# Optimization experiments

Hardware: AMD Instinct MI355X
Metric: run time of the kernel (lower is better)

## Reference

```python
import jax, jax.numpy as jnp
import numpy as np
import math

B, TQ, TK, C, H, DFF = 4, 1024, 1024, 1024, 16, 4096
DK = C // H
EPS = 1e-12


def _mha(x_q, x_kv, wq, bq, wk, bk, wv, bv, wo, bo, mask):
    Bq, Tq, Cq = x_q.shape
    Tk = x_kv.shape[1]
    q = (x_q @ wq + bq).reshape(Bq, Tq, H, DK).transpose(0, 2, 1, 3)  # [B,H,Tq,dk]
    k = (x_kv @ wk + bk).reshape(Bq, Tk, H, DK).transpose(0, 2, 1, 3)
    v = (x_kv @ wv + bv).reshape(Bq, Tk, H, DK).transpose(0, 2, 1, 3)
    scores = jnp.einsum('bhqd,bhkd->bhqk', q, k) * (1.0 / math.sqrt(DK))
    if mask is not None:
        scores = jnp.where(mask, scores, jnp.asarray(-1e9, scores.dtype))
    attn = jax.nn.softmax(scores, axis=-1)
    o = jnp.einsum('bhqk,bhkd->bhqd', attn, v).transpose(0, 2, 1, 3).reshape(Bq, Tq, Cq)
    return o @ wo + bo


def _ln(x, g, b):
    mu = jnp.mean(x, axis=-1, keepdims=True)
    var = jnp.mean(jnp.square(x - mu), axis=-1, keepdims=True)
    return (x - mu) * jax.lax.rsqrt(var + EPS) * g + b


def setup_inputs() -> dict:
    key = jax.random.key(0)
    ks = iter(jax.random.split(key, 32))
    s = 0.02
    inp = {}
    inp['src'] = jax.random.normal(next(ks), (B, TK, C), jnp.float32)
    inp['dst'] = jax.random.normal(next(ks), (B, TQ, C), jnp.float32)
    inp['src_mask'] = jnp.ones((B, 1, 1, TK), dtype=bool)  # key-padding mask (all valid)
    inp['dst_mask'] = jnp.tril(jnp.ones((TQ, TQ), dtype=bool))[None, None]  # causal
    for p in ['sa', 'ca']:
        for n in ['wq', 'wk', 'wv', 'wo']:
            inp[f'{p}_{n}'] = jax.random.normal(next(ks), (C, C), jnp.float32) * s
        for n in ['bq', 'bk', 'bv', 'bo']:
            inp[f'{p}_{n}'] = jnp.zeros((C,), jnp.float32)
    inp['ffn_w1'] = jax.random.normal(next(ks), (C, DFF), jnp.float32) * s
    inp['ffn_b1'] = jnp.zeros((DFF,), jnp.float32)
    inp['ffn_w2'] = jax.random.normal(next(ks), (DFF, C), jnp.float32) * s
    inp['ffn_b2'] = jnp.zeros((C,), jnp.float32)
    for i in ['1', '2', '3']:
        inp[f'ln{i}_g'] = jnp.ones((C,), jnp.float32)
        inp[f'ln{i}_b'] = jnp.zeros((C,), jnp.float32)
    return inp


def reference(src, dst, src_mask, dst_mask,
              sa_wq, sa_wk, sa_wv, sa_wo, sa_bq, sa_bk, sa_bv, sa_bo,
              ca_wq, ca_wk, ca_wv, ca_wo, ca_bq, ca_bk, ca_bv, ca_bo,
              ffn_w1, ffn_b1, ffn_w2, ffn_b2,
              ln1_g, ln1_b, ln2_g, ln2_b, ln3_g, ln3_b):
    # post-LN decoder layer, eval mode (dropout is identity)
    sa = _mha(dst, dst, sa_wq, sa_bq, sa_wk, sa_bk, sa_wv, sa_bv, sa_wo, sa_bo, dst_mask)
    y = _ln(dst + sa, ln1_g, ln1_b)
    ca = _mha(y, src, ca_wq, ca_bq, ca_wk, ca_bk, ca_wv, ca_bv, ca_wo, ca_bo, src_mask)
    y = _ln(y + ca, ln2_g, ln2_b)
    ff = jax.nn.gelu(y @ ffn_w1 + ffn_b1, approximate=False) @ ffn_w2 + ffn_b2
    return _ln(y + ff, ln3_g, ln3_b)
```

## Files before the change

### kernel.cpp

```cpp
#include <hip/hip_runtime.h>
#include <math.h>

typedef __attribute__((ext_vector_type(4))) float f32x4;
typedef __attribute__((ext_vector_type(8))) __bf16 bf16x8;
typedef __attribute__((ext_vector_type(8))) short short8;

#define DEV __device__ __forceinline__

DEV short f2bfs(float f) {
    unsigned u = __builtin_bit_cast(unsigned, f);
    unsigned r = (u + 0x7FFFu + ((u >> 16) & 1u)) >> 16;
    return (short)r;
}

DEV f32x4 mfma16(bf16x8 a, bf16x8 b, f32x4 c) {
    return __builtin_amdgcn_mfma_f32_16x16x32_bf16(a, b, c, 0, 0, 0);
}

DEV void gload_lds16(const void* g, void* l) {
    __builtin_amdgcn_global_load_lds((const __attribute__((address_space(1))) void*)g,
                                     (__attribute__((address_space(3))) void*)l, 16, 0, 0);
}

__global__ __launch_bounds__(256) void wtrans(const float* __restrict__ Win,
                                              short* __restrict__ Wout,
                                              int Kd, int Nd) {
    __shared__ float Tt[32][33];
    const int tx = threadIdx.x & 31, ty = threadIdx.x >> 5;
    const int k0 = blockIdx.y * 32, n0 = blockIdx.x * 32;
#pragma unroll
    for (int rr = 0; rr < 4; ++rr) {
        int k = ty * 4 + rr;
        Tt[k][tx] = Win[(size_t)(k0 + k) * Nd + n0 + tx];
    }
    __syncthreads();
#pragma unroll
    for (int rr = 0; rr < 4; ++rr) {
        int n = ty * 4 + rr;
        Wout[(size_t)(n0 + n) * Kd + k0 + tx] = f2bfs(Tt[tx][n]);
    }
}

struct WPtrs { const float* p[8]; };

__global__ __launch_bounds__(256) void wtrans8(WPtrs wp, short* __restrict__ out) {
    const float* __restrict__ Win = wp.p[blockIdx.z];
    short* __restrict__ Wout = out + (size_t)blockIdx.z * (1024 * 1024);
    __shared__ float Tt[32][33];
    const int tx = threadIdx.x & 31, ty = threadIdx.x >> 5;
    const int k0 = blockIdx.y * 32, n0 = blockIdx.x * 32;
#pragma unroll
    for (int rr = 0; rr < 4; ++rr) {
        int k = ty * 4 + rr;
        Tt[k][tx] = Win[(size_t)(k0 + k) * 1024 + n0 + tx];
    }
    __syncthreads();
#pragma unroll
    for (int rr = 0; rr < 4; ++rr) {
        int n = ty * 4 + rr;
        Wout[(size_t)(n0 + n) * 1024 + k0 + tx] = f2bfs(Tt[tx][n]);
    }
}

__global__ __launch_bounds__(256) void conv_bf16(const float* __restrict__ X,
                                                 short* __restrict__ Y, int n4) {
    int i = blockIdx.x * 256 + threadIdx.x;
    if (i < n4) {
        float4 v = ((const float4*)X)[i];
        short4 o;
        o.x = f2bfs(v.x); o.y = f2bfs(v.y); o.z = f2bfs(v.z); o.w = f2bfs(v.w);
        ((short4*)Y)[i] = o;
    }
}

template <int BM, int EPI>
__global__ __launch_bounds__(256) void gemm_bt(const short* __restrict__ A,
                                               const short* __restrict__ BT,
                                               const float* __restrict__ b0,
                                               const float* __restrict__ b1,
                                               const float* __restrict__ b2,
                                               void* __restrict__ o0,
                                               void* __restrict__ o1,
                                               void* __restrict__ o2,
                                               int M, int N, int K) {
    constexpr int IM = BM / 32;
    __shared__ __align__(16) short As[2][BM * 32];
    __shared__ __align__(16) short Bs[2][128 * 32];
    const int tid = threadIdx.x, lane = tid & 63, w = tid >> 6;
    const int m0 = blockIdx.y * BM, n0 = blockIdx.x * 128;
    const int wm = (w & 1) * (BM / 2), wn = (w >> 1) * 64;
    const int rl = lane & 15, rg = lane >> 4;
    f32x4 acc[IM][4] = {};
    const char* Ab = (const char*)A;
    const char* Bb = (const char*)BT;
    const int nk = K >> 5;

    auto stage = [&](int kt, int buf) {
#pragma unroll
        for (int r = 0; r < BM / 64; ++r) {
            int lo = (tid + r * 256) * 16;
            int row = lo >> 6, cp = (lo >> 4) & 3, c = (cp - row) & 3;
            gload_lds16(Ab + ((size_t)(m0 + row) * K + kt * 32 + c * 8) * 2,
                        (char*)As[buf] + lo);
        }
#pragma unroll
        for (int r = 0; r < 2; ++r) {
            int lo = (tid + r * 256) * 16;
            int row = lo >> 6, cp = (lo >> 4) & 3, c = (cp - row) & 3;
            gload_lds16(Bb + ((size_t)(n0 + row) * K + kt * 32 + c * 8) * 2,
                        (char*)Bs[buf] + lo);
        }
    };

    stage(0, 0);
    for (int kt = 0; kt < nk; ++kt) {
        const int buf = kt & 1;
        __syncthreads();
        if (kt + 1 < nk) stage(kt + 1, buf ^ 1);
        bf16x8 af[IM], bfr[4];
#pragma unroll
        for (int i = 0; i < IM; i++) {
            int row = wm + i * 16 + rl;
            af[i] = *(const bf16x8*)(As[buf] + row * 32 + ((rg + row) & 3) * 8);
        }
#pragma unroll
        for (int j = 0; j < 4; j++) {
            int row = wn + j * 16 + rl;
            bfr[j] = *(const bf16x8*)(Bs[buf] + row * 32 + ((rg + row) & 3) * 8);
        }
#pragma unroll
        for (int i = 0; i < IM; i++)
#pragma unroll
            for (int j = 0; j < 4; j++)
                acc[i][j] = mfma16(af[i], bfr[j], acc[i][j]);
    }

#pragma unroll
    for (int i = 0; i < IM; i++) {
        int gm0 = m0 + wm + i * 16 + rg * 4;
#pragma unroll
        for (int j = 0; j < 4; j++) {
            int gn = n0 + wn + j * 16 + rl;
            if (EPI == 0) {
                float bv = b0[gn];
#pragma unroll
                for (int r = 0; r < 4; r++)
                    ((float*)o0)[(size_t)(gm0 + r) * N + gn] = acc[i][j][r] + bv;
            } else if (EPI == 2) {
                float bv = b0[gn];
#pragma unroll
                for (int r = 0; r < 4; r++) {
                    float x = acc[i][j][r] + bv;
                    float z = 1.59576912f * x + 0.07135481f * x * x * x;
                    float g = x / (1.0f + __expf(-z));
                    ((short*)o0)[(size_t)(gm0 + r) * N + gn] = f2bfs(g);
                }
            } else {
                int seg = gn >> 10, n1 = gn & 1023, h = n1 >> 6, d = n1 & 63;
                int b = gm0 >> 10, t0 = gm0 & 1023;
                bool isV = (EPI == 1) ? (seg == 2) : (seg == 1);
                const float* bp = (EPI == 1) ? (seg == 0 ? b0 : (seg == 1 ? b1 : b2))
                                             : (seg == 0 ? b0 : b1);
                float bv = bp[n1];
                float qs = (EPI == 1 && seg == 0) ? 0.125f : 1.0f;
                if (!isV) {
                    short* hp = (short*)((EPI == 1) ? (seg == 0 ? o0 : o1) : o0);
                    size_t base = ((size_t)(b * 16 + h) * 1024 + t0) * 64 + d;
#pragma unroll
                    for (int r = 0; r < 4; r++)
                        hp[base + (size_t)r * 64] = f2bfs((acc[i][j][r] + bv) * qs);
                } else {
                    short* vp = (short*)((EPI == 1) ? o2 : o1);
                    short4 pk;
                    pk.x = f2bfs(acc[i][j][0] + bv);
                    pk.y = f2bfs(acc[i][j][1] + bv);
                    pk.z = f2bfs(acc[i][j][2] + bv);
                    pk.w = f2bfs(acc[i][j][3] + bv);
                    *(short4*)(vp + ((size_t)(b * 16 + h) * 64 + d) * 1024 + t0) = pk;
                }
            }
        }
    }
}

template <bool CAUSAL>
__global__ __launch_bounds__(256, 3) void attn4(const short* __restrict__ Qh,
                                                const short* __restrict__ Kh,
                                                const short* __restrict__ VTh,
                                                short* __restrict__ Out, int TKn) {
    __shared__ __align__(16) short Ks[2][64 * 64];
    __shared__ __align__(16) short Vts[2][64 * 64];
    __shared__ __align__(16) short Ps[4][16 * 72 + 8];
    const int tid = threadIdx.x, lane = tid & 63, w = tid >> 6;
    const int rl = lane & 15, rg = lane >> 4;
    const int bh = blockIdx.y, b = bh >> 4, h = bh & 15;
    const int q0 = blockIdx.x * 64;
    const short* Qp = Qh + (size_t)bh * 1024 * 64;
    const char* Kp = (const char*)(Kh + (size_t)bh * (size_t)TKn * 64);
    const char* Vp = (const char*)(VTh + (size_t)bh * (size_t)TKn * 64);

    const int qrow = q0 + w * 16 + rl;
    const bf16x8 qf0 = *(const bf16x8*)(Qp + (size_t)qrow * 64 + rg * 8);
    const bf16x8 qf1 = *(const bf16x8*)(Qp + (size_t)qrow * 64 + 32 + rg * 8);

    bf16x8 onesf;
#pragma unroll
    for (int i = 0; i < 8; ++i) onesf[i] = (__bf16)1.0f;

    f32x4 o[4] = {};
    f32x4 lacc = {};

    short* Pw = &Ps[w][0];
    const int nkt = CAUSAL ? blockIdx.x + 1 : (TKn >> 6);

    auto stage = [&](int kt, int buf) {
#pragma unroll
        for (int r = 0; r < 2; ++r) {
            int lo = (w * 2 + r) * 1024 + lane * 16;
            int row = lo >> 7, cp = (lo >> 4) & 7, c = (cp - row) & 7;
            gload_lds16(Kp + ((size_t)(kt * 64 + row) * 64 + c * 8) * 2,
                        (char*)Ks[buf] + lo);
            gload_lds16(Vp + ((size_t)row * TKn + kt * 64 + c * 8) * 2,
                        (char*)Vts[buf] + lo);
        }
    };

    stage(0, 0);
    for (int kt = 0; kt < nkt; ++kt) {
        const int buf = kt & 1;
        __syncthreads();
        if (kt + 1 < nkt) stage(kt + 1, buf ^ 1);

        const short* KsB = Ks[buf];
        f32x4 s[4];
#pragma unroll
        for (int ch = 0; ch < 4; ++ch) {
            int row = ch * 16 + rl;
            bf16x8 k0 = *(const bf16x8*)(KsB + row * 64 + ((rg + row) & 7) * 8);
            bf16x8 k1 = *(const bf16x8*)(KsB + row * 64 + ((rg + 4 + row) & 7) * 8);
            f32x4 z = {};
            z = mfma16(k0, qf0, z);
            z = mfma16(k1, qf1, z);
            s[ch] = z;
        }
        const bool domask = CAUSAL && (kt == nkt - 1);
#pragma unroll
        for (int ch = 0; ch < 4; ++ch) {
            float p[4];
#pragma unroll
            for (int r = 0; r < 4; ++r) {
                float e = __expf(s[ch][r]);
                if (domask) {
                    int key = kt * 64 + ch * 16 + rg * 4 + r;
                    if (key > qrow) e = 0.0f;
                }
                p[r] = e;
            }
            unsigned d0 = (__builtin_bit_cast(unsigned, p[1]) & 0xFFFF0000u) |
                          (__builtin_bit_cast(unsigned, p[0]) >> 16);
            unsigned d1 = (__builtin_bit_cast(unsigned, p[3]) & 0xFFFF0000u) |
                          (__builtin_bit_cast(unsigned, p[2]) >> 16);
            uint2 dv; dv.x = d0; dv.y = d1;
            *(uint2*)(Pw + rl * 72 + ch * 16 + rg * 4) = dv;
        }
        bf16x8 pa0 = *(const bf16x8*)(Pw + rl * 72 + rg * 8);
        bf16x8 pa1 = *(const bf16x8*)(Pw + rl * 72 + 32 + rg * 8);
        lacc = mfma16(pa0, onesf, lacc);
        lacc = mfma16(pa1, onesf, lacc);
        const short* VsB = Vts[buf];
#pragma unroll
        for (int j = 0; j < 4; ++j) {
            int row = j * 16 + rl;
            bf16x8 v0 = *(const bf16x8*)(VsB + row * 64 + ((rg + row) & 7) * 8);
            bf16x8 v1 = *(const bf16x8*)(VsB + row * 64 + ((rg + 4 + row) & 7) * 8);
            o[j] = mfma16(pa0, v0, o[j]);
            o[j] = mfma16(pa1, v1, o[j]);
        }
    }

    float inv[4];
#pragma unroll
    for (int r = 0; r < 4; r++) inv[r] = 1.0f / lacc[r];
#pragma unroll
    for (int j = 0; j < 4; j++) {
#pragma unroll
        for (int r = 0; r < 4; r++) {
            int row = q0 + w * 16 + rg * 4 + r;
            int col = h * 64 + j * 16 + rl;
            Out[((size_t)b * 1024 + row) * 1024 + col] = f2bfs(o[j][r] * inv[r]);
        }
    }
}

__global__ __launch_bounds__(256) void ln_fused(const float* __restrict__ X,
                                                const float* __restrict__ R,
                                                const float* __restrict__ gam,
                                                const float* __restrict__ bet,
                                                float* __restrict__ Yf,
                                                short* __restrict__ Yb) {
    const int row = blockIdx.x, tid = threadIdx.x;
    const int lane = tid & 63, w = tid >> 6;
    const float* xr = X + (size_t)row * 1024;
    const float* rr = R + (size_t)row * 1024;
    float4 xv = ((const float4*)xr)[tid];
    float4 rv = ((const float4*)rr)[tid];
    float v0 = xv.x + rv.x, v1 = xv.y + rv.y, v2 = xv.z + rv.z, v3 = xv.w + rv.w;
    float s = v0 + v1 + v2 + v3;
    float ss = v0 * v0 + v1 * v1 + v2 * v2 + v3 * v3;
#pragma unroll
    for (int off = 1; off < 64; off <<= 1) {
        s += __shfl_xor(s, off);
        ss += __shfl_xor(ss, off);
    }
    __shared__ float sred[4], ssred[4];
    if (lane == 0) { sred[w] = s; ssred[w] = ss; }
    __syncthreads();
    s = sred[0] + sred[1] + sred[2] + sred[3];
    ss = ssred[0] + ssred[1] + ssred[2] + ssred[3];
    float mu = s * (1.0f / 1024.0f);
    float var = ss * (1.0f / 1024.0f) - mu * mu;
    float rsq = rsqrtf(var + 1e-12f);
    float4 gv = ((const float4*)gam)[tid];
    float4 bv = ((const float4*)bet)[tid];
    float y0 = (v0 - mu) * rsq * gv.x + bv.x;
    float y1 = (v1 - mu) * rsq * gv.y + bv.y;
    float y2 = (v2 - mu) * rsq * gv.z + bv.z;
    float y3 = (v3 - mu) * rsq * gv.w + bv.w;
    float4 yo = {y0, y1, y2, y3};
    ((float4*)(Yf + (size_t)row * 1024))[tid] = yo;
    if (Yb) {
        short4 ob;
        ob.x = f2bfs(y0); ob.y = f2bfs(y1); ob.z = f2bfs(y2); ob.w = f2bfs(y3);
        ((short4*)(Yb + (size_t)row * 1024))[tid] = ob;
    }
}

extern "C" void kernel_launch(void* const* d_in, const int* in_sizes, int n_in,
                              void* d_out, int out_size, void* d_ws, size_t ws_size,
                              hipStream_t stream) {
    const float* src = (const float*)d_in[0];
    const float* dst = (const float*)d_in[1];
    const float* sa_wq = (const float*)d_in[4];
    const float* sa_wk = (const float*)d_in[5];
    const float* sa_wv = (const float*)d_in[6];
    const float* sa_wo = (const float*)d_in[7];
    const float* sa_bq = (const float*)d_in[8];
    const float* sa_bk = (const float*)d_in[9];
    const float* sa_bv = (const float*)d_in[10];
    const float* sa_bo = (const float*)d_in[11];
    const float* ca_wq = (const float*)d_in[12];
    const float* ca_wk = (const float*)d_in[13];
    const float* ca_wv = (const float*)d_in[14];
    const float* ca_wo = (const float*)d_in[15];
    const float* ca_bq = (const float*)d_in[16];
    const float* ca_bk = (const float*)d_in[17];
    const float* ca_bv = (const float*)d_in[18];
    const float* ca_bo = (const float*)d_in[19];
    const float* ffn_w1 = (const float*)d_in[20];
    const float* ffn_b1 = (const float*)d_in[21];
    const float* ffn_w2 = (const float*)d_in[22];
    const float* ffn_b2 = (const float*)d_in[23];
    const float* ln1g = (const float*)d_in[24];
    const float* ln1b = (const float*)d_in[25];
    const float* ln2g = (const float*)d_in[26];
    const float* ln2b = (const float*)d_in[27];
    const float* ln3g = (const float*)d_in[28];
    const float* ln3b = (const float*)d_in[29];

    char* ws = (char*)d_ws;
    size_t off = 0;
    auto alloc = [&](size_t n) { size_t o = off; off = (off + n + 255) & ~(size_t)255; return o; };

    const size_t szW = (size_t)1024 * 1024 * 2;
    short* wT = (short*)(ws + alloc(8 * szW));
    short* w1T = (short*)(ws + alloc((size_t)4096 * 1024 * 2));
    short* w2T = (short*)(ws + alloc((size_t)1024 * 4096 * 2));
    const size_t szAct2 = (size_t)4096 * 1024 * 2;
    const size_t szAct4 = (size_t)4096 * 1024 * 4;
    short* dstb = (short*)(ws + alloc(szAct2));
    short* srcb = (short*)(ws + alloc(szAct2));
    short* Qh = (short*)(ws + alloc(szAct2));
    short* Kh = (short*)(ws + alloc(szAct2));
    short* VTh = (short*)(ws + alloc(szAct2));
    short* attnb = (short*)(ws + alloc(szAct2));
    float* tmp = (float*)(ws + alloc(szAct4));
    float* y1f = (float*)(ws + alloc(szAct4));
    short* y1b = (short*)(ws + alloc(szAct2));
    float* y2f = (float*)(ws + alloc(szAct4));
    short* y2b = (short*)(ws + alloc(szAct2));
    short* ffnh = (short*)(ws + alloc((size_t)4096 * 4096 * 2));

    short* sa_wqkvT = wT;
    short* sa_woT = wT + 3 * (size_t)1048576;
    short* ca_wqT = wT + 4 * (size_t)1048576;
    short* ca_wkvT = wT + 5 * (size_t)1048576;
    short* ca_woT = wT + 7 * (size_t)1048576;

    dim3 blk(256);

    WPtrs wp = {{sa_wq, sa_wk, sa_wv, sa_wo, ca_wq, ca_wk, ca_wv, ca_wo}};
    wtrans8<<<dim3(32, 32, 8), blk, 0, stream>>>(wp, wT);
    wtrans<<<dim3(128, 32), blk, 0, stream>>>(ffn_w1, w1T, 1024, 4096);
    wtrans<<<dim3(32, 128), blk, 0, stream>>>(ffn_w2, w2T, 4096, 1024);
    conv_bf16<<<4096, blk, 0, stream>>>(dst, dstb, 1048576);
    conv_bf16<<<4096, blk, 0, stream>>>(src, srcb, 1048576);

    gemm_bt<128, 1><<<dim3(24, 32), blk, 0, stream>>>(dstb, sa_wqkvT, sa_bq, sa_bk, sa_bv,
                                                      Qh, Kh, VTh, 4096, 3072, 1024);
    attn4<true><<<dim3(16, 64), blk, 0, stream>>>(Qh, Kh, VTh, attnb, 1024);
    gemm_bt<64, 0><<<dim3(8, 64), blk, 0, stream>>>(attnb, sa_woT, sa_bo, nullptr, nullptr,
                                                    tmp, nullptr, nullptr, 4096, 1024, 1024);
    ln_fused<<<4096, blk, 0, stream>>>(dst, tmp, ln1g, ln1b, y1f, y1b);

    gemm_bt<64, 1><<<dim3(8, 64), blk, 0, stream>>>(y1b, ca_wqT, ca_bq, nullptr, nullptr,
                                                    Qh, nullptr, nullptr, 4096, 1024, 1024);
    gemm_bt<128, 3><<<dim3(16, 32), blk, 0, stream>>>(srcb, ca_wkvT, ca_bk, ca_bv, nullptr,
                                                      Kh, VTh, nullptr, 4096, 2048, 1024);
    attn4<false><<<dim3(16, 64), blk, 0, stream>>>(Qh, Kh, VTh, attnb, 1024);
    gemm_bt<64, 0><<<dim3(8, 64), blk, 0, stream>>>(attnb, ca_woT, ca_bo, nullptr, nullptr,
                                                    tmp, nullptr, nullptr, 4096, 1024, 1024);
    ln_fused<<<4096, blk, 0, stream>>>(y1f, tmp, ln2g, ln2b, y2f, y2b);

    gemm_bt<128, 2><<<dim3(32, 32), blk, 0, stream>>>(y2b, w1T, ffn_b1, nullptr, nullptr,
                                                      ffnh, nullptr, nullptr, 4096, 4096, 1024);
    gemm_bt<64, 0><<<dim3(8, 64), blk, 0, stream>>>(ffnh, w2T, ffn_b2, nullptr, nullptr,
                                                    tmp, nullptr, nullptr, 4096, 1024, 4096);
    ln_fused<<<4096, blk, 0, stream>>>(y2f, tmp, ln3g, ln3b, (float*)d_out, nullptr);

    (void)in_sizes; (void)n_in; (void)out_size; (void)ws_size;
}
```

Measured before the change: 544.1 us.

## Split-K the N=1024 output GEMMs and fold partial sums into LayerNorm

The three output-projection GEMMs (N=1024) now run with a two-way split over K via blockIdx.z. Each half writes its partial result to a separate fp32 buffer, and the bias is added only in the first half. The following LayerNorm kernel reads both partials and sums them into the residual, so no separate reduction kernel is needed. This doubles the block count for GEMMs that launched only 512 blocks, to fill more CUs, at the cost of writing and reading an extra fp32 activation buffer. The LDS swizzle also changes from (row) to (row>>1), which alters the bank-conflict pattern of the tile loads and reads.

```diff
diff --git a/kernel.cpp b/kernel.cpp
--- a/kernel.cpp
+++ b/kernel.cpp
@@ -82,12 +82,13 @@
                                                void* __restrict__ o0,
                                                void* __restrict__ o1,
                                                void* __restrict__ o2,
-                                               int M, int N, int K) {
+                                               int M, int N, int K, int Ks) {
     constexpr int IM = BM / 32;
     __shared__ __align__(16) short As[2][BM * 32];
     __shared__ __align__(16) short Bs[2][128 * 32];
     const int tid = threadIdx.x, lane = tid & 63, w = tid >> 6;
     const int m0 = blockIdx.y * BM, n0 = blockIdx.x * 128;
+    const int kz = blockIdx.z * K;
     const int wm = (w & 1) * (BM / 2), wn = (w >> 1) * 64;
     const int rl = lane & 15, rg = lane >> 4;
     f32x4 acc[IM][4] = {};
@@ -99,15 +100,15 @@
 #pragma unroll
         for (int r = 0; r < BM / 64; ++r) {
             int lo = (tid + r * 256) * 16;
-            int row = lo >> 6, cp = (lo >> 4) & 3, c = (cp - row) & 3;
-            gload_lds16(Ab + ((size_t)(m0 + row) * K + kt * 32 + c * 8) * 2,
+            int row = lo >> 6, cp = (lo >> 4) & 3, c = (cp - (row >> 1)) & 3;
+            gload_lds16(Ab + ((size_t)(m0 + row) * Ks + kz + kt * 32 + c * 8) * 2,
                         (char*)As[buf] + lo);
         }
 #pragma unroll
         for (int r = 0; r < 2; ++r) {
             int lo = (tid + r * 256) * 16;
-            int row = lo >> 6, cp = (lo >> 4) & 3, c = (cp - row) & 3;
-            gload_lds16(Bb + ((size_t)(n0 + row) * K + kt * 32 + c * 8) * 2,
+            int row = lo >> 6, cp = (lo >> 4) & 3, c = (cp - (row >> 1)) & 3;
+            gload_lds16(Bb + ((size_t)(n0 + row) * Ks + kz + kt * 32 + c * 8) * 2,
                         (char*)Bs[buf] + lo);
         }
     };
@@ -121,12 +122,12 @@
 #pragma unroll
         for (int i = 0; i < IM; i++) {
             int row = wm + i * 16 + rl;
-            af[i] = *(const bf16x8*)(As[buf] + row * 32 + ((rg + row) & 3) * 8);
+            af[i] = *(const bf16x8*)(As[buf] + row * 32 + ((rg + (row >> 1)) & 3) * 8);
         }
 #pragma unroll
         for (int j = 0; j < 4; j++) {
             int row = wn + j * 16 + rl;
-            bfr[j] = *(const bf16x8*)(Bs[buf] + row * 32 + ((rg + row) & 3) * 8);
+            bfr[j] = *(const bf16x8*)(Bs[buf] + row * 32 + ((rg + (row >> 1)) & 3) * 8);
         }
 #pragma unroll
         for (int i = 0; i < IM; i++)
@@ -135,6 +136,7 @@
                 acc[i][j] = mfma16(af[i], bfr[j], acc[i][j]);
     }
 
+    float* o0z = (float*)o0 + (size_t)blockIdx.z * M * N;
 #pragma unroll
     for (int i = 0; i < IM; i++) {
         int gm0 = m0 + wm + i * 16 + rg * 4;
@@ -142,10 +144,10 @@
         for (int j = 0; j < 4; j++) {
             int gn = n0 + wn + j * 16 + rl;
             if (EPI == 0) {
-                float bv = b0[gn];
+                float bv = blockIdx.z == 0 ? b0[gn] : 0.0f;
 #pragma unroll
                 for (int r = 0; r < 4; r++)
-                    ((float*)o0)[(size_t)(gm0 + r) * N + gn] = acc[i][j][r] + bv;
+                    o0z[(size_t)(gm0 + r) * N + gn] = acc[i][j][r] + bv;
             } else if (EPI == 2) {
                 float bv = b0[gn];
 #pragma unroll
@@ -294,17 +296,20 @@
 
 __global__ __launch_bounds__(256) void ln_fused(const float* __restrict__ X,
                                                 const float* __restrict__ R,
+                                                const float* __restrict__ R2,
                                                 const float* __restrict__ gam,
                                                 const float* __restrict__ bet,
                                                 float* __restrict__ Yf,
                                                 short* __restrict__ Yb) {
     const int row = blockIdx.x, tid = threadIdx.x;
     const int lane = tid & 63, w = tid >> 6;
-    const float* xr = X + (size_t)row * 1024;
-    const float* rr = R + (size_t)row * 1024;
-    float4 xv = ((const float4*)xr)[tid];
-    float4 rv = ((const float4*)rr)[tid];
+    float4 xv = ((const float4*)(X + (size_t)row * 1024))[tid];
+    float4 rv = ((const float4*)(R + (size_t)row * 1024))[tid];
     float v0 = xv.x + rv.x, v1 = xv.y + rv.y, v2 = xv.z + rv.z, v3 = xv.w + rv.w;
+    if (R2) {
+        float4 r2 = ((const float4*)(R2 + (size_t)row * 1024))[tid];
+        v0 += r2.x; v1 += r2.y; v2 += r2.z; v3 += r2.w;
+    }
     float s = v0 + v1 + v2 + v3;
     float ss = v0 * v0 + v1 * v1 + v2 * v2 + v3 * v3;
 #pragma unroll
@@ -383,7 +388,8 @@
     short* Kh = (short*)(ws + alloc(szAct2));
     short* VTh = (short*)(ws + alloc(szAct2));
     short* attnb = (short*)(ws + alloc(szAct2));
-    float* tmp = (float*)(ws + alloc(szAct4));
+    float* tmp = (float*)(ws + alloc(2 * szAct4));
+    float* tmp2 = tmp + (size_t)4096 * 1024;
     float* y1f = (float*)(ws + alloc(szAct4));
     short* y1b = (short*)(ws + alloc(szAct2));
     float* y2f = (float*)(ws + alloc(szAct4));
@@ -406,26 +412,26 @@
     conv_bf16<<<4096, blk, 0, stream>>>(src, srcb, 1048576);
 
     gemm_bt<128, 1><<<dim3(24, 32), blk, 0, stream>>>(dstb, sa_wqkvT, sa_bq, sa_bk, sa_bv,
-                                                      Qh, Kh, VTh, 4096, 3072, 1024);
+                                                      Qh, Kh, VTh, 4096, 3072, 1024, 1024);
     attn4<true><<<dim3(16, 64), blk, 0, stream>>>(Qh, Kh, VTh, attnb, 1024);
-    gemm_bt<64, 0><<<dim3(8, 64), blk, 0, stream>>>(attnb, sa_woT, sa_bo, nullptr, nullptr,
-                                                    tmp, nullptr, nullptr, 4096, 1024, 1024);
-    ln_fused<<<4096, blk, 0, stream>>>(dst, tmp, ln1g, ln1b, y1f, y1b);
+    gemm_bt<64, 0><<<dim3(8, 64, 2), blk, 0, stream>>>(attnb, sa_woT, sa_bo, nullptr, nullptr,
+                                                       tmp, nullptr, nullptr, 4096, 1024, 512, 1024);
+    ln_fused<<<4096, blk, 0, stream>>>(dst, tmp, tmp2, ln1g, ln1b, y1f, y1b);
 
     gemm_bt<64, 1><<<dim3(8, 64), blk, 0, stream>>>(y1b, ca_wqT, ca_bq, nullptr, nullptr,
-                                                    Qh, nullptr, nullptr, 4096, 1024, 1024);
+                                                    Qh, nullptr, nullptr, 4096, 1024, 1024, 1024);
     gemm_bt<128, 3><<<dim3(16, 32), blk, 0, stream>>>(srcb, ca_wkvT, ca_bk, ca_bv, nullptr,
-                                                      Kh, VTh, nullptr, 4096, 2048, 1024);
+                                                      Kh, VTh, nullptr, 4096, 2048, 1024, 1024);
     attn4<false><<<dim3(16, 64), blk, 0, stream>>>(Qh, Kh, VTh, attnb, 1024);
-    gemm_bt<64, 0><<<dim3(8, 64), blk, 0, stream>>>(attnb, ca_woT, ca_bo, nullptr, nullptr,
-                                                    tmp, nullptr, nullptr, 4096, 1024, 1024);
-    ln_fused<<<4096, blk, 0, stream>>>(y1f, tmp, ln2g, ln2b, y2f, y2b);
+    gemm_bt<64, 0><<<dim3(8, 64, 2), blk, 0, stream>>>(attnb, ca_woT, ca_bo, nullptr, nullptr,
+                                                       tmp, nullptr, nullptr, 4096, 1024, 512, 1024);
+    ln_fused<<<4096, blk, 0, stream>>>(y1f, tmp, tmp2, ln2g, ln2b, y2f, y2b);
 
     gemm_bt<128, 2><<<dim3(32, 32), blk, 0, stream>>>(y2b, w1T, ffn_b1, nullptr, nullptr,
-                                                      ffnh, nullptr, nullptr, 4096, 4096, 1024);
-    gemm_bt<64, 0><<<dim3(8, 64), blk, 0, stream>>>(ffnh, w2T, ffn_b2, nullptr, nullptr,
-                                                    tmp, nullptr, nullptr, 4096, 1024, 4096);
-    ln_fused<<<4096, blk, 0, stream>>>(y2f, tmp, ln3g, ln3b, (float*)d_out, nullptr);
+                                                      ffnh, nullptr, nullptr, 4096, 4096, 1024, 1024);
+    gemm_bt<64, 0><<<dim3(8, 64, 2), blk, 0, stream>>>(ffnh, w2T, ffn_b2, nullptr, nullptr,
+                                                       tmp, nullptr, nullptr, 4096, 1024, 2048, 4096);
+    ln_fused<<<4096, blk, 0, stream>>>(y2f, tmp, tmp2, ln3g, ln3b, (float*)d_out, nullptr);
 
     (void)in_sizes; (void)n_in; (void)out_size; (void)ws_size;
 }
```

Measured after the change: 541.1 us. Within noise of the previous version (-0.6%).
